# Optimization experiments

Hardware: AMD Instinct MI355X
Metric: run time of the kernel (lower is better)

Reference implementation:

```python
import jax, jax.numpy as jnp
import numpy as np
import math

B, H, W = 32, 512, 512
BS = 8
QUALITY = 50.0  # __scale_quality(75) = 200 - 2*75


def _make_dctmtx(bs=BS):
    m = np.empty((bs, bs), dtype=np.float32)
    for j in range(bs):
        for i in range(bs):
            if i == 0:
                m[i, j] = 1.0 / math.sqrt(bs)
            else:
                m[i, j] = math.sqrt(2.0 / bs) * math.cos(math.pi * (2 * j + 1) * i / (2 * bs))
    return jnp.asarray(m)


def _make_quantize():
    qY = np.array([[16,11,10,16,24,40,51,61],[12,12,14,19,26,58,60,55],
                   [14,13,16,24,40,57,69,56],[14,17,22,29,51,87,80,62],
                   [18,22,37,56,68,109,103,77],[24,35,55,64,81,104,113,92],
                   [49,64,78,87,103,121,120,101],[72,92,95,98,112,100,103,99]], dtype=np.float32) / 255.0
    qC = np.array([[17,18,24,47,99,99,99,99],[18,21,26,66,99,99,99,99],
                   [24,26,56,99,99,99,99,99],[47,66,99,99,99,99,99,99],
                   [99,99,99,99,99,99,99,99],[99,99,99,99,99,99,99,99],
                   [99,99,99,99,99,99,99,99],[99,99,99,99,99,99,99,99]], dtype=np.float32) / 255.0
    return jnp.asarray(np.stack([qY, qC, qC], axis=0))


def setup_inputs() -> dict:
    key = jax.random.key(0)
    x = jax.random.uniform(key, (B, 3, H, W), dtype=jnp.float32)
    return {"input": x, "quantize": _make_quantize(), "dctmtx": _make_dctmtx()}


def reference(input, quantize, dctmtx):
    bs = BS
    b, c, h, w = input.shape
    dt = input.dtype
    rgb = 255.0 * input
    # rgb -> ycbcr (3x3 color transform, offset cb/cr by 128, clamp)
    xf = jnp.array([[0.299, 0.587, 0.114],
                    [-0.168735892, -0.331264108, 0.5],
                    [0.5, -0.418687589, -0.081312411]], dtype=dt)
    off = jnp.array([0.0, 128.0, 128.0], dtype=dt)[None, :, None, None]
    ycbcr = jnp.clip(jnp.einsum('bchw,kc->bkhw', rgb, xf) + off, 0.0, 255.0)
    # 2x2 chroma subsample: replace Cb/Cr by 2x2 block means (Y untouched)
    yc = ycbcr[:, :1]
    cc = ycbcr[:, 1:].reshape(b, 2, h // 2, 2, w // 2, 2)
    cm = jnp.mean(cc, axis=(3, 5), keepdims=True)
    cc = jnp.broadcast_to(cm, cc.shape).reshape(b, 2, h, w)
    sample = jnp.concatenate([yc, cc], axis=1) - 128.0
    # extract 8x8 blocks -> [b, h/bs, w/bs, 3, bs, bs]
    blocks = sample.reshape(b, 3, h // bs, bs, w // bs, bs).transpose(0, 2, 4, 1, 3, 5)
    # 2D DCT: D @ X @ D^T
    dcts = jnp.einsum('ij,bhwcjk,lk->bhwcil', dctmtx, blocks, dctmtx)
    # quality-scaled quant table (broadcasts [3,8,8] over blocks)
    q = jnp.round(jnp.clip(jnp.round((jnp.round(quantize * 255.0) * QUALITY + 50.0) / 100.0), 1.0, 255.0))
    comp = jnp.round(dcts / q)
    decomp = jnp.round(comp * jax.lax.stop_gradient(q))
    # IDCT: D^T @ X @ D
    idcts = jnp.einsum('ji,bhwcjk,kl->bhwcil', dctmtx, decomp, dctmtx)
    # merge blocks back -> [b,3,h,w]
    ycbcr2 = idcts.transpose(0, 3, 1, 4, 2, 5).reshape(b, 3, h, w) + 128.0
    # ycbcr -> rgb
    xf2 = jnp.array([[1.0, 0.0, 1.402],
                     [1.0, -0.344136286, -0.714136286],
                     [1.0, 1.772, 0.0]], dtype=dt)
    im = ycbcr2 - off
    rgb2 = jnp.clip(jnp.einsum('bchw,kc->bkhw', im, xf2), 0.0, 255.0)
    return jnp.round(rgb2) / 255.0
```

## Files before the change

kernel.cpp:

```cpp
#include <hip/hip_runtime.h>

#define IN_H 512
#define IN_W 512


__global__ __launch_bounds__(256, 5) void jpeg_kernel(
    const float* __restrict__ in, const float* __restrict__ qz,
    const float* __restrict__ dmtx, float* __restrict__ out)
{
    __shared__ __align__(16) unsigned char smem[30464];
    double*  Ys  = (double*) (smem);
    double*  CbS = (double*) (smem + 17408);
    double*  CrS = (double*) (smem + 22016);
    double2* qt  = (double2*)(smem + 26624);
    double*  Dd  = (double*) (smem + 30080);
    float*   Dh  = (float*)  (smem + 30336);

    const int t   = threadIdx.x;
    const int blk = blockIdx.x;
    const int b   = blk >> 7;
    const int rr  = blk & 127;
    const int row0 = (rr >> 1) << 3;
    const int col0 = (rr & 1) << 8;
    const int chs = IN_H * IN_W;

    if (t < 192) {
        const int c = t >> 6, i = (t >> 3) & 7, l = t & 7;
        double v  = (double)qz[t];
        double t1 = rint((rint(v * 255.0) * 50.0 + 50.0) / 100.0);
        double q  = fmin(fmax(t1, 1.0), 255.0);
        qt[(c * 8 + l) * 9 + i] = make_double2(1.0 / q, q);
    }
    if (t < 32) {
        float dv = dmtx[(t >> 2) * 8 + (t & 3)];
        Dd[t] = (double)dv;
        Dh[t] = dv;
    }

    const int s  = t >> 6;
    const int c4 = t & 63;
    {
        const int base = ((b * 3) * IN_H + row0 + 2 * s) * IN_W + col0 + 4 * c4;
        float4 ra = *(const float4*)(in + base);
        float4 rb = *(const float4*)(in + base + IN_W);
        float4 ga = *(const float4*)(in + base + chs);
        float4 gb = *(const float4*)(in + base + chs + IN_W);
        float4 ba = *(const float4*)(in + base + 2 * chs);
        float4 bb = *(const float4*)(in + base + 2 * chs + IN_W);

        float rA[2][4] = {{ra.x,ra.y,ra.z,ra.w},{rb.x,rb.y,rb.z,rb.w}};
        float gA[2][4] = {{ga.x,ga.y,ga.z,ga.w},{gb.x,gb.y,gb.z,gb.w}};
        float bA[2][4] = {{ba.x,ba.y,ba.z,ba.w},{bb.x,bb.y,bb.z,bb.w}};

        double yv[2][4], cbv[2][4], crv[2][4];
        #pragma unroll
        for (int p = 0; p < 2; ++p) {
            #pragma unroll
            for (int k = 0; k < 4; ++k) {
                double R = 255.0 * (double)rA[p][k];
                double G = 255.0 * (double)gA[p][k];
                double B = 255.0 * (double)bA[p][k];
                double y  =  0.299*R + 0.587*G + 0.114*B;
                double cb = -0.168735892*R - 0.331264108*G + 0.5*B + 128.0;
                double cr =  0.5*R - 0.418687589*G - 0.081312411*B + 128.0;
                yv[p][k]  = fmin(fmax(y , 0.0), 255.0) - 128.0;
                cbv[p][k] = fmin(fmax(cb, 0.0), 255.0);
                crv[p][k] = fmin(fmax(cr, 0.0), 255.0);
            }
        }
        const int tile = c4 >> 1, half = c4 & 1;
        #pragma unroll
        for (int p = 0; p < 2; ++p) {
            double* yp = &Ys[tile * 68 + (2*s + p) * 8 + 4 * half];
            *(double2*)(yp)     = make_double2(yv[p][0], yv[p][1]);
            *(double2*)(yp + 2) = make_double2(yv[p][2], yv[p][3]);
        }
        double m0 = (cbv[0][0]+cbv[0][1]+cbv[1][0]+cbv[1][1])*0.25 - 128.0;
        double m1 = (cbv[0][2]+cbv[0][3]+cbv[1][2]+cbv[1][3])*0.25 - 128.0;
        *(double2*)&CbS[tile * 18 + s * 4 + 2 * half] = make_double2(m0, m1);
        double n0 = (crv[0][0]+crv[0][1]+crv[1][0]+crv[1][1])*0.25 - 128.0;
        double n1 = (crv[0][2]+crv[0][3]+crv[1][2]+crv[1][3])*0.25 - 128.0;
        *(double2*)&CrS[tile * 18 + s * 4 + 2 * half] = make_double2(n0, n1);
    }
    __syncthreads();

    const int q8 = t >> 3;
    const int l  = t & 7;
    double dl0, dl1, dl2, dl3;
    {
        double2 dA = *(const double2*)&Dd[l * 4];
        double2 dB = *(const double2*)&Dd[l * 4 + 2];
        dl0 = dA.x; dl1 = dA.y; dl2 = dB.x; dl3 = dB.y;
    }
    const double sgn  = (l & 1) ? -1.0 : 1.0;
    const double dl01 = dl0 + dl1, dl23 = dl2 + dl3;
    const float4* dh4p = (const float4*)Dh;
    float4 d0 = dh4p[0], d1 = dh4p[1], d2 = dh4p[2], d3 = dh4p[3];
    float4 d4 = dh4p[4], d5 = dh4p[5], d6 = dh4p[6], d7 = dh4p[7];

    float acc[3][8];
    float* vtw = (float*)(smem + q8 * 544 + 272);

    #pragma unroll
    for (int c = 0; c < 3; ++c) {
        double e2[4], o2[4];
        if (c == 0) {
            const double* base = &Ys[q8 * 68];
            #pragma unroll
            for (int m = 0; m < 4; ++m) {
                double tp[2];
                #pragma unroll
                for (int h = 0; h < 2; ++h) {
                    const double* p = base + (h ? (7 - m) : m) * 8;
                    double2 a0 = *(const double2*)(p);
                    double2 a1 = *(const double2*)(p + 2);
                    double2 a2 = *(const double2*)(p + 4);
                    double2 a3 = *(const double2*)(p + 6);
                    double v0 = fma(sgn, a3.y, a0.x);
                    double v1 = fma(sgn, a3.x, a0.y);
                    double v2 = fma(sgn, a2.y, a1.x);
                    double v3 = fma(sgn, a2.x, a1.y);
                    tp[h] = dl0*v0 + dl1*v1 + dl2*v2 + dl3*v3;
                }
                e2[m] = tp[0] + tp[1];
                o2[m] = tp[0] - tp[1];
            }
        } else {
            const double* base = ((c == 1) ? CbS : CrS) + q8 * 18;
            double u4[4];
            #pragma unroll
            for (int j2 = 0; j2 < 4; ++j2) {
                double2 a0 = *(const double2*)(base + j2 * 4);
                double2 a1 = *(const double2*)(base + j2 * 4 + 2);
                u4[j2] = dl01 * fma(sgn, a1.y, a0.x) + dl23 * fma(sgn, a1.x, a0.y);
            }
            e2[0] = e2[1] = u4[0] + u4[3];  o2[0] = o2[1] = u4[0] - u4[3];
            e2[2] = e2[3] = u4[1] + u4[2];  o2[2] = o2[3] = u4[1] - u4[2];
        }

        float zo[8];
        {
            const double2* dd2  = (const double2*)Dd;
            const double2* qrow = &qt[(c * 8 + l) * 9];
            #pragma unroll
            for (int i = 0; i < 8; ++i) {
                double2 dA = dd2[i * 2], dB = dd2[i * 2 + 1];
                double a64 = (i & 1)
                    ? dA.x*o2[0] + dA.y*o2[1] + dB.x*o2[2] + dB.y*o2[3]
                    : dA.x*e2[0] + dA.y*e2[1] + dB.x*e2[2] + dB.y*e2[3];
                double2 qe = qrow[i];
                zo[i] = (float)(rint(a64 * qe.x) * qe.y);
            }
        }

        float u[8];
        {
            float se0 = zo[0]*d0.x + zo[2]*d2.x + zo[4]*d4.x + zo[6]*d6.x;
            float se1 = zo[0]*d0.y + zo[2]*d2.y + zo[4]*d4.y + zo[6]*d6.y;
            float se2 = zo[0]*d0.z + zo[2]*d2.z + zo[4]*d4.z + zo[6]*d6.z;
            float se3 = zo[0]*d0.w + zo[2]*d2.w + zo[4]*d4.w + zo[6]*d6.w;
            float so0 = zo[1]*d1.x + zo[3]*d3.x + zo[5]*d5.x + zo[7]*d7.x;
            float so1 = zo[1]*d1.y + zo[3]*d3.y + zo[5]*d5.y + zo[7]*d7.y;
            float so2 = zo[1]*d1.z + zo[3]*d3.z + zo[5]*d5.z + zo[7]*d7.z;
            float so3 = zo[1]*d1.w + zo[3]*d3.w + zo[5]*d5.w + zo[7]*d7.w;
            u[0]=se0+so0; u[7]=se0-so0;
            u[1]=se1+so1; u[6]=se1-so1;
            u[2]=se2+so2; u[5]=se2-so2;
            u[3]=se3+so3; u[4]=se3-so3;
        }

        __builtin_amdgcn_wave_barrier();
        #pragma unroll
        for (int x = 0; x < 8; ++x) vtw[x * 8 + l] = u[x];
        __builtin_amdgcn_wave_barrier();
        float w2[8];
        {
            const float* vr = vtw + l * 8;
            float4 wa = *(const float4*)(vr);
            float4 wb = *(const float4*)(vr + 4);
            w2[0]=wa.x; w2[1]=wa.y; w2[2]=wa.z; w2[3]=wa.w;
            w2[4]=wb.x; w2[5]=wb.y; w2[6]=wb.z; w2[7]=wb.w;
        }
        __builtin_amdgcn_wave_barrier();

        {
            float re0 = w2[0]*d0.x + w2[2]*d2.x + w2[4]*d4.x + w2[6]*d6.x;
            float re1 = w2[0]*d0.y + w2[2]*d2.y + w2[4]*d4.y + w2[6]*d6.y;
            float re2 = w2[0]*d0.z + w2[2]*d2.z + w2[4]*d4.z + w2[6]*d6.z;
            float re3 = w2[0]*d0.w + w2[2]*d2.w + w2[4]*d4.w + w2[6]*d6.w;
            float ro0 = w2[1]*d1.x + w2[3]*d3.x + w2[5]*d5.x + w2[7]*d7.x;
            float ro1 = w2[1]*d1.y + w2[3]*d3.y + w2[5]*d5.y + w2[7]*d7.y;
            float ro2 = w2[1]*d1.z + w2[3]*d3.z + w2[5]*d5.z + w2[7]*d7.z;
            float ro3 = w2[1]*d1.w + w2[3]*d3.w + w2[5]*d5.w + w2[7]*d7.w;
            acc[c][0]=re0+ro0; acc[c][7]=re0-ro0;
            acc[c][1]=re1+ro1; acc[c][6]=re1-ro1;
            acc[c][2]=re2+ro2; acc[c][5]=re2-ro2;
            acc[c][3]=re3+ro3; acc[c][4]=re3-ro3;
        }
    }

    {
        const int obase = ((b * 3) * IN_H + row0 + l) * IN_W + col0 + q8 * 8;
        float R4[8], G4[8], B4[8];
        #pragma unroll
        for (int y = 0; y < 8; ++y) {
            float im0 = acc[0][y] + 128.0f;
            float im1 = acc[1][y];
            float im2 = acc[2][y];
            float R  = fminf(fmaxf(im0 + 1.402f*im2, 0.0f), 255.0f);
            float G  = fminf(fmaxf(im0 - 0.344136286f*im1 - 0.714136286f*im2, 0.0f), 255.0f);
            float Bv = fminf(fmaxf(im0 + 1.772f*im1, 0.0f), 255.0f);
            R4[y] = rintf(R)  * (1.0f/255.0f);
            G4[y] = rintf(G)  * (1.0f/255.0f);
            B4[y] = rintf(Bv) * (1.0f/255.0f);
        }
        *(float4*)(out + obase)               = make_float4(R4[0],R4[1],R4[2],R4[3]);
        *(float4*)(out + obase + 4)           = make_float4(R4[4],R4[5],R4[6],R4[7]);
        *(float4*)(out + obase + chs)         = make_float4(G4[0],G4[1],G4[2],G4[3]);
        *(float4*)(out + obase + chs + 4)     = make_float4(G4[4],G4[5],G4[6],G4[7]);
        *(float4*)(out + obase + 2*chs)       = make_float4(B4[0],B4[1],B4[2],B4[3]);
        *(float4*)(out + obase + 2*chs + 4)   = make_float4(B4[4],B4[5],B4[6],B4[7]);
    }
}

extern "C" void kernel_launch(void* const* d_in, const int* in_sizes, int n_in,
                              void* d_out, int out_size, void* d_ws, size_t ws_size,
                              hipStream_t stream) {
    (void)in_sizes; (void)n_in; (void)out_size; (void)d_ws; (void)ws_size;
    const float* in  = (const float*)d_in[0];
    const float* qz  = (const float*)d_in[1];
    const float* dm  = (const float*)d_in[2];
    float* out = (float*)d_out;
    dim3 grid(4096), blk(256);
    hipLaunchKernelGGL(jpeg_kernel, grid, blk, 0, stream, in, qz, dm, out);
}
```

Baseline: 187.3 us.

## Share Y-channel row DCT across lanes via shared memory instead of recomputing

```diff
diff --git a/kernel.cpp b/kernel.cpp
--- a/kernel.cpp
+++ b/kernel.cpp
@@ -4,17 +4,17 @@
 #define IN_W 512
 
 
-__global__ __launch_bounds__(256, 5) void jpeg_kernel(
+__global__ __launch_bounds__(256, 2) void jpeg_kernel(
     const float* __restrict__ in, const float* __restrict__ qz,
     const float* __restrict__ dmtx, float* __restrict__ out)
 {
-    __shared__ __align__(16) unsigned char smem[30464];
+    __shared__ __align__(16) unsigned char smem[30976];
     double*  Ys  = (double*) (smem);
-    double*  CbS = (double*) (smem + 17408);
-    double*  CrS = (double*) (smem + 22016);
-    double2* qt  = (double2*)(smem + 26624);
-    double*  Dd  = (double*) (smem + 30080);
-    float*   Dh  = (float*)  (smem + 30336);
+    double*  CbS = (double*) (smem + 17920);
+    double*  CrS = (double*) (smem + 22528);
+    double2* qt  = (double2*)(smem + 27136);
+    double*  Dd  = (double*) (smem + 30592);
+    float*   Dh  = (float*)  (smem + 30848);
 
     const int t   = threadIdx.x;
     const int blk = blockIdx.x;
@@ -71,7 +71,7 @@
         const int tile = c4 >> 1, half = c4 & 1;
         #pragma unroll
         for (int p = 0; p < 2; ++p) {
-            double* yp = &Ys[tile * 68 + (2*s + p) * 8 + 4 * half];
+            double* yp = &Ys[tile * 70 + (2*s + p) * 8 + 4 * half];
             *(double2*)(yp)     = make_double2(yv[p][0], yv[p][1]);
             *(double2*)(yp + 2) = make_double2(yv[p][2], yv[p][3]);
         }
@@ -99,31 +99,43 @@
     float4 d4 = dh4p[4], d5 = dh4p[5], d6 = dh4p[6], d7 = dh4p[7];
 
     float acc[3][8];
-    float* vtw = (float*)(smem + q8 * 544 + 272);
+    float* vtw = (float*)(smem + q8 * 560 + 272);
 
     #pragma unroll
     for (int c = 0; c < 3; ++c) {
         double e2[4], o2[4];
         if (c == 0) {
-            const double* base = &Ys[q8 * 68];
+            double* rowp = &Ys[q8 * 70 + l * 8];
+            {
+                double2 a0 = *(const double2*)(rowp);
+                double2 a1 = *(const double2*)(rowp + 2);
+                double2 a2 = *(const double2*)(rowp + 4);
+                double2 a3 = *(const double2*)(rowp + 6);
+                double ev0 = a0.x + a3.y, ov0 = a0.x - a3.y;
+                double ev1 = a0.y + a3.x, ov1 = a0.y - a3.x;
+                double ev2 = a1.x + a2.y, ov2 = a1.x - a2.y;
+                double ev3 = a1.y + a2.x, ov3 = a1.y - a2.x;
+                double g0v = (double)d0.x*ev0 + (double)d0.y*ev1 + (double)d0.z*ev2 + (double)d0.w*ev3;
+                double g1v = (double)d1.x*ov0 + (double)d1.y*ov1 + (double)d1.z*ov2 + (double)d1.w*ov3;
+                double g2v = (double)d2.x*ev0 + (double)d2.y*ev1 + (double)d2.z*ev2 + (double)d2.w*ev3;
+                double g3v = (double)d3.x*ov0 + (double)d3.y*ov1 + (double)d3.z*ov2 + (double)d3.w*ov3;
+                double g4v = (double)d4.x*ev0 + (double)d4.y*ev1 + (double)d4.z*ev2 + (double)d4.w*ev3;
+                double g5v = (double)d5.x*ov0 + (double)d5.y*ov1 + (double)d5.z*ov2 + (double)d5.w*ov3;
+                double g6v = (double)d6.x*ev0 + (double)d6.y*ev1 + (double)d6.z*ev2 + (double)d6.w*ev3;
+                double g7v = (double)d7.x*ov0 + (double)d7.y*ov1 + (double)d7.z*ov2 + (double)d7.w*ov3;
+                *(double2*)(rowp)     = make_double2(g0v, g1v);
+                *(double2*)(rowp + 2) = make_double2(g2v, g3v);
+                *(double2*)(rowp + 4) = make_double2(g4v, g5v);
+                *(double2*)(rowp + 6) = make_double2(g6v, g7v);
+            }
+            __builtin_amdgcn_wave_barrier();
+            const double* tb = &Ys[q8 * 70 + l];
             #pragma unroll
             for (int m = 0; m < 4; ++m) {
-                double tp[2];
-                #pragma unroll
-                for (int h = 0; h < 2; ++h) {
-                    const double* p = base + (h ? (7 - m) : m) * 8;
-                    double2 a0 = *(const double2*)(p);
-                    double2 a1 = *(const double2*)(p + 2);
-                    double2 a2 = *(const double2*)(p + 4);
-                    double2 a3 = *(const double2*)(p + 6);
-                    double v0 = fma(sgn, a3.y, a0.x);
-                    double v1 = fma(sgn, a3.x, a0.y);
-                    double v2 = fma(sgn, a2.y, a1.x);
-                    double v3 = fma(sgn, a2.x, a1.y);
-                    tp[h] = dl0*v0 + dl1*v1 + dl2*v2 + dl3*v3;
-                }
-                e2[m] = tp[0] + tp[1];
-                o2[m] = tp[0] - tp[1];
+                double gm = tb[m * 8];
+                double g7 = tb[(7 - m) * 8];
+                e2[m] = gm + g7;
+                o2[m] = gm - g7;
             }
         } else {
             const double* base = ((c == 1) ? CbS : CrS) + q8 * 18;
```

After: 184.7 us. About the same (-1.4%).

## Remap color-stage threads per tile and replace block barrier with wave barrier

Applied to the files above, without the earlier changes.

```diff
diff --git a/kernel.cpp b/kernel.cpp
--- a/kernel.cpp
+++ b/kernel.cpp
@@ -4,7 +4,7 @@
 #define IN_W 512
 
 
-__global__ __launch_bounds__(256, 5) void jpeg_kernel(
+__global__ __launch_bounds__(256, 2) void jpeg_kernel(
     const float* __restrict__ in, const float* __restrict__ qz,
     const float* __restrict__ dmtx, float* __restrict__ out)
 {
@@ -24,6 +24,18 @@
     const int col0 = (rr & 1) << 8;
     const int chs = IN_H * IN_W;
 
+    const int tile = t >> 3;
+    const int h4   = (t >> 2) & 1;
+    const int s    = t & 3;
+
+    const int base = ((b * 3) * IN_H + row0 + 2 * s) * IN_W + col0 + tile * 8 + 4 * h4;
+    float4 ra = *(const float4*)(in + base);
+    float4 rb = *(const float4*)(in + base + IN_W);
+    float4 ga = *(const float4*)(in + base + chs);
+    float4 gb = *(const float4*)(in + base + chs + IN_W);
+    float4 ba = *(const float4*)(in + base + 2 * chs);
+    float4 bb = *(const float4*)(in + base + 2 * chs + IN_W);
+
     if (t < 192) {
         const int c = t >> 6, i = (t >> 3) & 7, l = t & 7;
         double v  = (double)qz[t];
@@ -36,18 +48,9 @@
         Dd[t] = (double)dv;
         Dh[t] = dv;
     }
-
-    const int s  = t >> 6;
-    const int c4 = t & 63;
-    {
-        const int base = ((b * 3) * IN_H + row0 + 2 * s) * IN_W + col0 + 4 * c4;
-        float4 ra = *(const float4*)(in + base);
-        float4 rb = *(const float4*)(in + base + IN_W);
-        float4 ga = *(const float4*)(in + base + chs);
-        float4 gb = *(const float4*)(in + base + chs + IN_W);
-        float4 ba = *(const float4*)(in + base + 2 * chs);
-        float4 bb = *(const float4*)(in + base + 2 * chs + IN_W);
-
+    __syncthreads();
+
+    {
         float rA[2][4] = {{ra.x,ra.y,ra.z,ra.w},{rb.x,rb.y,rb.z,rb.w}};
         float gA[2][4] = {{ga.x,ga.y,ga.z,ga.w},{gb.x,gb.y,gb.z,gb.w}};
         float bA[2][4] = {{ba.x,ba.y,ba.z,ba.w},{bb.x,bb.y,bb.z,bb.w}};
@@ -68,21 +71,20 @@
                 crv[p][k] = fmin(fmax(cr, 0.0), 255.0);
             }
         }
-        const int tile = c4 >> 1, half = c4 & 1;
         #pragma unroll
         for (int p = 0; p < 2; ++p) {
-            double* yp = &Ys[tile * 68 + (2*s + p) * 8 + 4 * half];
+            double* yp = &Ys[tile * 68 + (2*s + p) * 8 + 4 * h4];
             *(double2*)(yp)     = make_double2(yv[p][0], yv[p][1]);
             *(double2*)(yp + 2) = make_double2(yv[p][2], yv[p][3]);
         }
         double m0 = (cbv[0][0]+cbv[0][1]+cbv[1][0]+cbv[1][1])*0.25 - 128.0;
         double m1 = (cbv[0][2]+cbv[0][3]+cbv[1][2]+cbv[1][3])*0.25 - 128.0;
-        *(double2*)&CbS[tile * 18 + s * 4 + 2 * half] = make_double2(m0, m1);
+        *(double2*)&CbS[tile * 18 + s * 4 + 2 * h4] = make_double2(m0, m1);
         double n0 = (crv[0][0]+crv[0][1]+crv[1][0]+crv[1][1])*0.25 - 128.0;
         double n1 = (crv[0][2]+crv[0][3]+crv[1][2]+crv[1][3])*0.25 - 128.0;
-        *(double2*)&CrS[tile * 18 + s * 4 + 2 * half] = make_double2(n0, n1);
-    }
-    __syncthreads();
+        *(double2*)&CrS[tile * 18 + s * 4 + 2 * h4] = make_double2(n0, n1);
+    }
+    __builtin_amdgcn_wave_barrier();
 
     const int q8 = t >> 3;
     const int l  = t & 7;
@@ -94,110 +96,111 @@
     }
     const double sgn  = (l & 1) ? -1.0 : 1.0;
     const double dl01 = dl0 + dl1, dl23 = dl2 + dl3;
+
+    double e20[4], o20[4];
+    {
+        const double* basep = &Ys[q8 * 68];
+        #pragma unroll
+        for (int m = 0; m < 4; ++m) {
+            double tp[2];
+            #pragma unroll
+            for (int hh = 0; hh < 2; ++hh) {
+                const double* p = basep + (hh ? (7 - m) : m) * 8;
+                double2 a0 = *(const double2*)(p);
+                double2 a1 = *(const double2*)(p + 2);
+                double2 a2 = *(const double2*)(p + 4);
+                double2 a3 = *(const double2*)(p + 6);
+                double v0 = fma(sgn, a3.y, a0.x);
+                double v1 = fma(sgn, a3.x, a0.y);
+                double v2 = fma(sgn, a2.y, a1.x);
+                double v3 = fma(sgn, a2.x, a1.y);
+                tp[hh] = dl0*v0 + dl1*v1 + dl2*v2 + dl3*v3;
+            }
+            e20[m] = tp[0] + tp[1];
+            o20[m] = tp[0] - tp[1];
+        }
+    }
+    double e21[4], o21[4], e22[4], o22[4];
+    #pragma unroll
+    for (int cc = 0; cc < 2; ++cc) {
+        const double* basep = (cc == 0 ? CbS : CrS) + q8 * 18;
+        double u4[4];
+        #pragma unroll
+        for (int j2 = 0; j2 < 4; ++j2) {
+            double2 a0 = *(const double2*)(basep + j2 * 4);
+            double2 a1 = *(const double2*)(basep + j2 * 4 + 2);
+            u4[j2] = dl01 * fma(sgn, a1.y, a0.x) + dl23 * fma(sgn, a1.x, a0.y);
+        }
+        double ea = u4[0] + u4[3], oa = u4[0] - u4[3];
+        double eb = u4[1] + u4[2], ob = u4[1] - u4[2];
+        if (cc == 0) { e21[0]=e21[1]=ea; o21[0]=o21[1]=oa; e21[2]=e21[3]=eb; o21[2]=o21[3]=ob; }
+        else         { e22[0]=e22[1]=ea; o22[0]=o22[1]=oa; e22[2]=e22[3]=eb; o22[2]=o22[3]=ob; }
+    }
+
+    float zo[3][8];
+    {
+        const double2* dd2 = (const double2*)Dd;
+        #pragma unroll
+        for (int i = 0; i < 8; ++i) {
+            double2 dA = dd2[i * 2], dB = dd2[i * 2 + 1];
+            #define ZQ(C, E, O) { \
+                double a64 = (i & 1) \
+                    ? dA.x*O[0] + dA.y*O[1] + dB.x*O[2] + dB.y*O[3] \
+                    : dA.x*E[0] + dA.y*E[1] + dB.x*E[2] + dB.y*E[3]; \
+                double2 qe = qt[(C * 8 + l) * 9 + i]; \
+                zo[C][i] = (float)(rint(a64 * qe.x) * qe.y); }
+            ZQ(0, e20, o20)
+            ZQ(1, e21, o21)
+            ZQ(2, e22, o22)
+            #undef ZQ
+        }
+    }
+
     const float4* dh4p = (const float4*)Dh;
     float4 d0 = dh4p[0], d1 = dh4p[1], d2 = dh4p[2], d3 = dh4p[3];
     float4 d4 = dh4p[4], d5 = dh4p[5], d6 = dh4p[6], d7 = dh4p[7];
 
     float acc[3][8];
-    float* vtw = (float*)(smem + q8 * 544 + 272);
-
-    #pragma unroll
-    for (int c = 0; c < 3; ++c) {
-        double e2[4], o2[4];
-        if (c == 0) {
-            const double* base = &Ys[q8 * 68];
-            #pragma unroll
-            for (int m = 0; m < 4; ++m) {
-                double tp[2];
-                #pragma unroll
-                for (int h = 0; h < 2; ++h) {
-                    const double* p = base + (h ? (7 - m) : m) * 8;
-                    double2 a0 = *(const double2*)(p);
-                    double2 a1 = *(const double2*)(p + 2);
-                    double2 a2 = *(const double2*)(p + 4);
-                    double2 a3 = *(const double2*)(p + 6);
-                    double v0 = fma(sgn, a3.y, a0.x);
-                    double v1 = fma(sgn, a3.x, a0.y);
-                    double v2 = fma(sgn, a2.y, a1.x);
-                    double v3 = fma(sgn, a2.x, a1.y);
-                    tp[h] = dl0*v0 + dl1*v1 + dl2*v2 + dl3*v3;
-                }
-                e2[m] = tp[0] + tp[1];
-                o2[m] = tp[0] - tp[1];
-            }
-        } else {
-            const double* base = ((c == 1) ? CbS : CrS) + q8 * 18;
-            double u4[4];
-            #pragma unroll
-            for (int j2 = 0; j2 < 4; ++j2) {
-                double2 a0 = *(const double2*)(base + j2 * 4);
-                double2 a1 = *(const double2*)(base + j2 * 4 + 2);
-                u4[j2] = dl01 * fma(sgn, a1.y, a0.x) + dl23 * fma(sgn, a1.x, a0.y);
-            }
-            e2[0] = e2[1] = u4[0] + u4[3];  o2[0] = o2[1] = u4[0] - u4[3];
-            e2[2] = e2[3] = u4[1] + u4[2];  o2[2] = o2[3] = u4[1] - u4[2];
-        }
-
-        float zo[8];
-        {
-            const double2* dd2  = (const double2*)Dd;
-            const double2* qrow = &qt[(c * 8 + l) * 9];
-            #pragma unroll
-            for (int i = 0; i < 8; ++i) {
-                double2 dA = dd2[i * 2], dB = dd2[i * 2 + 1];
-                double a64 = (i & 1)
-                    ? dA.x*o2[0] + dA.y*o2[1] + dB.x*o2[2] + dB.y*o2[3]
-                    : dA.x*e2[0] + dA.y*e2[1] + dB.x*e2[2] + dB.y*e2[3];
-                double2 qe = qrow[i];
-                zo[i] = (float)(rint(a64 * qe.x) * qe.y);
-            }
-        }
-
-        float u[8];
-        {
-            float se0 = zo[0]*d0.x + zo[2]*d2.x + zo[4]*d4.x + zo[6]*d6.x;
-            float se1 = zo[0]*d0.y + zo[2]*d2.y + zo[4]*d4.y + zo[6]*d6.y;
-            float se2 = zo[0]*d0.z + zo[2]*d2.z + zo[4]*d4.z + zo[6]*d6.z;
-            float se3 = zo[0]*d0.w + zo[2]*d2.w + zo[4]*d4.w + zo[6]*d6.w;
-            float so0 = zo[1]*d1.x + zo[3]*d3.x + zo[5]*d5.x + zo[7]*d7.x;
-            float so1 = zo[1]*d1.y + zo[3]*d3.y + zo[5]*d5.y + zo[7]*d7.y;
-            float so2 = zo[1]*d1.z + zo[3]*d3.z + zo[5]*d5.z + zo[7]*d7.z;
-            float so3 = zo[1]*d1.w + zo[3]*d3.w + zo[5]*d5.w + zo[7]*d7.w;
-            u[0]=se0+so0; u[7]=se0-so0;
-            u[1]=se1+so1; u[6]=se1-so1;
-            u[2]=se2+so2; u[5]=se2-so2;
-            u[3]=se3+so3; u[4]=se3-so3;
-        }
-
-        __builtin_amdgcn_wave_barrier();
-        #pragma unroll
-        for (int x = 0; x < 8; ++x) vtw[x * 8 + l] = u[x];
-        __builtin_amdgcn_wave_barrier();
-        float w2[8];
-        {
-            const float* vr = vtw + l * 8;
-            float4 wa = *(const float4*)(vr);
-            float4 wb = *(const float4*)(vr + 4);
-            w2[0]=wa.x; w2[1]=wa.y; w2[2]=wa.z; w2[3]=wa.w;
-            w2[4]=wb.x; w2[5]=wb.y; w2[6]=wb.z; w2[7]=wb.w;
-        }
-        __builtin_amdgcn_wave_barrier();
-
-        {
-            float re0 = w2[0]*d0.x + w2[2]*d2.x + w2[4]*d4.x + w2[6]*d6.x;
-            float re1 = w2[0]*d0.y + w2[2]*d2.y + w2[4]*d4.y + w2[6]*d6.y;
-            float re2 = w2[0]*d0.z + w2[2]*d2.z + w2[4]*d4.z + w2[6]*d6.z;
-            float re3 = w2[0]*d0.w + w2[2]*d2.w + w2[4]*d4.w + w2[6]*d6.w;
-            float ro0 = w2[1]*d1.x + w2[3]*d3.x + w2[5]*d5.x + w2[7]*d7.x;
-            float ro1 = w2[1]*d1.y + w2[3]*d3.y + w2[5]*d5.y + w2[7]*d7.y;
-            float ro2 = w2[1]*d1.z + w2[3]*d3.z + w2[5]*d5.z + w2[7]*d7.z;
-            float ro3 = w2[1]*d1.w + w2[3]*d3.w + w2[5]*d5.w + w2[7]*d7.w;
-            acc[c][0]=re0+ro0; acc[c][7]=re0-ro0;
-            acc[c][1]=re1+ro1; acc[c][6]=re1-ro1;
-            acc[c][2]=re2+ro2; acc[c][5]=re2-ro2;
-            acc[c][3]=re3+ro3; acc[c][4]=re3-ro3;
-        }
-    }
+    float* vtwA = (float*)(smem + q8 * 544);
+    float* vtwB = (float*)(smem + q8 * 544 + 288);
+
+    #define EPI(C, VT) { \
+        float se0 = zo[C][0]*d0.x + zo[C][2]*d2.x + zo[C][4]*d4.x + zo[C][6]*d6.x; \
+        float se1 = zo[C][0]*d0.y + zo[C][2]*d2.y + zo[C][4]*d4.y + zo[C][6]*d6.y; \
+        float se2 = zo[C][0]*d0.z + zo[C][2]*d2.z + zo[C][4]*d4.z + zo[C][6]*d6.z; \
+        float se3 = zo[C][0]*d0.w + zo[C][2]*d2.w + zo[C][4]*d4.w + zo[C][6]*d6.w; \
+        float so0 = zo[C][1]*d1.x + zo[C][3]*d3.x + zo[C][5]*d5.x + zo[C][7]*d7.x; \
+        float so1 = zo[C][1]*d1.y + zo[C][3]*d3.y + zo[C][5]*d5.y + zo[C][7]*d7.y; \
+        float so2 = zo[C][1]*d1.z + zo[C][3]*d3.z + zo[C][5]*d5.z + zo[C][7]*d7.z; \
+        float so3 = zo[C][1]*d1.w + zo[C][3]*d3.w + zo[C][5]*d5.w + zo[C][7]*d7.w; \
+        float u0 = se0+so0, u7 = se0-so0; \
+        float u1 = se1+so1, u6 = se1-so1; \
+        float u2 = se2+so2, u5 = se2-so2; \
+        float u3 = se3+so3, u4v = se3-so3; \
+        __builtin_amdgcn_wave_barrier(); \
+        VT[0*8+l]=u0; VT[1*8+l]=u1; VT[2*8+l]=u2; VT[3*8+l]=u3; \
+        VT[4*8+l]=u4v; VT[5*8+l]=u5; VT[6*8+l]=u6; VT[7*8+l]=u7; \
+        __builtin_amdgcn_wave_barrier(); \
+        float4 wa = *(const float4*)(VT + l * 8); \
+        float4 wb = *(const float4*)(VT + l * 8 + 4); \
+        __builtin_amdgcn_wave_barrier(); \
+        float re0 = wa.x*d0.x + wa.z*d2.x + wb.x*d4.x + wb.z*d6.x; \
+        float re1 = wa.x*d0.y + wa.z*d2.y + wb.x*d4.y + wb.z*d6.y; \
+        float re2 = wa.x*d0.z + wa.z*d2.z + wb.x*d4.z + wb.z*d6.z; \
+        float re3 = wa.x*d0.w + wa.z*d2.w + wb.x*d4.w + wb.z*d6.w; \
+        float ro0 = wa.y*d1.x + wa.w*d3.x + wb.y*d5.x + wb.w*d7.x; \
+        float ro1 = wa.y*d1.y + wa.w*d3.y + wb.y*d5.y + wb.w*d7.y; \
+        float ro2 = wa.y*d1.z + wa.w*d3.z + wb.y*d5.z + wb.w*d7.z; \
+        float ro3 = wa.y*d1.w + wa.w*d3.w + wb.y*d5.w + wb.w*d7.w; \
+        acc[C][0]=re0+ro0; acc[C][7]=re0-ro0; \
+        acc[C][1]=re1+ro1; acc[C][6]=re1-ro1; \
+        acc[C][2]=re2+ro2; acc[C][5]=re2-ro2; \
+        acc[C][3]=re3+ro3; acc[C][4]=re3-ro3; }
+
+    EPI(0, vtwA)
+    EPI(1, vtwB)
+    EPI(2, vtwA)
+    #undef EPI
 
     {
         const int obase = ((b * 3) * IN_H + row0 + l) * IN_W + col0 + q8 * 8;
```

After: 181.5 us. -3.1%, faster.
